# Kernel optimization log

Hardware: AMD Instinct MI355X
Metric: run time of the kernel (lower is better)

The kernel has to match this reference:

```python
import jax, jax.numpy as jnp
import numpy as np
from jax import lax

# 8-neighbor zero-pad offsets as (left, right, top, bottom), matching nn.ZeroPad2d args
PADS = [(0, 2, 0, 2), (1, 1, 0, 2), (2, 0, 0, 2), (0, 2, 1, 1),
        (2, 0, 1, 1), (0, 2, 2, 0), (1, 1, 2, 0), (2, 0, 2, 0)]
BN_EPS = 1e-5


def conv2d(x, w, pad):
    return lax.conv_general_dilated(x, w, (1, 1), [(pad, pad), (pad, pad)],
                                    dimension_numbers=('NCHW', 'OIHW', 'NCHW'))


def batchnorm(x, gamma, beta, mean, var):
    inv = gamma * lax.rsqrt(var + BN_EPS)
    return x * inv[None, :, None, None] + (beta - mean * inv)[None, :, None, None]


def resize_bilinear(x, oh, ow):
    # F.interpolate(mode='bilinear', align_corners=False)
    n, c, h, w = x.shape
    ys = jnp.clip((jnp.arange(oh, dtype=x.dtype) + 0.5) * (h / oh) - 0.5, 0.0, None)
    xs = jnp.clip((jnp.arange(ow, dtype=x.dtype) + 0.5) * (w / ow) - 0.5, 0.0, None)
    y0 = jnp.floor(ys); x0 = jnp.floor(xs)
    wy = (ys - y0)[:, None]; wx = (xs - x0)[None, :]
    y0i = jnp.clip(y0.astype(jnp.int32), 0, h - 1)
    y1i = jnp.clip(y0i + 1, 0, h - 1)
    x0i = jnp.clip(x0.astype(jnp.int32), 0, w - 1)
    x1i = jnp.clip(x0i + 1, 0, w - 1)
    r0 = x[:, :, y0i, :]; r1 = x[:, :, y1i, :]
    top = r0[:, :, :, x0i] * (1 - wx) + r0[:, :, :, x1i] * wx
    bot = r1[:, :, :, x0i] * (1 - wx) + r1[:, :, :, x1i] * wx
    return top * (1 - wy) + bot * wy


def lrwarp_error(left, disp, right):
    # Warp right image toward left using horizontal disparity (bilinear,
    # zero padding outside), then per-channel absolute photometric error.
    n, c, h, w = right.shape
    xs = jnp.arange(w, dtype=disp.dtype)[None, None, None, :] - disp  # [n,1,h,w]
    x0 = jnp.floor(xs)
    frac = xs - x0
    x0i = x0.astype(jnp.int32)
    x1i = x0i + 1
    v0 = ((x0i >= 0) & (x0i < w)).astype(right.dtype)
    v1 = ((x1i >= 0) & (x1i < w)).astype(right.dtype)
    x0c = jnp.broadcast_to(jnp.clip(x0i, 0, w - 1), (n, c, h, w))
    x1c = jnp.broadcast_to(jnp.clip(x1i, 0, w - 1), (n, c, h, w))
    g0 = jnp.take_along_axis(right, x0c, axis=3) * v0
    g1 = jnp.take_along_axis(right, x1c, axis=3) * v1
    warped = g0 * (1 - frac) + g1 * frac
    return jnp.abs(left - warped)


def setup_inputs() -> dict:
    key = jax.random.key(0)
    ks = jax.random.split(key, 16)
    N, H, W = 8, 256, 256
    inp = {
        'normal_estimation': jax.random.normal(ks[0], (N, 3, H, W), jnp.float32),
        'left_image': jax.random.uniform(ks[1], (N, 3, 512, 512), jnp.float32),
        'right_image': jax.random.uniform(ks[2], (N, 3, 512, 512), jnp.float32),
        'coarse_disparity': jax.random.uniform(ks[3], (N, 1, H, W), jnp.float32),
        'w1': jax.random.normal(ks[4], (32, 12, 3, 3), jnp.float32) * 0.1,
        'g1': jnp.ones((32,), jnp.float32), 'b1': jnp.zeros((32,), jnp.float32),
        'm1': jax.random.normal(ks[5], (32,), jnp.float32) * 0.01,
        'v1': jax.random.uniform(ks[6], (32,), jnp.float32, 0.5, 1.5),
        'w2': jax.random.normal(ks[7], (64, 32, 3, 3), jnp.float32) * 0.1,
        'g2': jnp.ones((64,), jnp.float32), 'b2': jnp.zeros((64,), jnp.float32),
        'm2': jax.random.normal(ks[8], (64,), jnp.float32) * 0.01,
        'v2': jax.random.uniform(ks[9], (64,), jnp.float32, 0.5, 1.5),
        'w3': jax.random.normal(ks[10], (8, 64, 1, 1), jnp.float32) * 0.1,
    }
    return inp


def _forward(normal_estimation, left_image, right_image, coarse_disparity,
             w1, g1, b1, m1, v1, w2, g2, b2, m2, v2, w3):
    H, W = coarse_disparity.shape[-2], coarse_disparity.shape[-1]
    cur_l = resize_bilinear(left_image, H, W)
    cur_r = resize_bilinear(right_image, H, W)
    disp_err = lrwarp_error(cur_l, coarse_disparity, cur_r)
    feats = jnp.concatenate([normal_estimation, cur_l, cur_r, disp_err], axis=1)
    x = jax.nn.relu(batchnorm(conv2d(feats, w1, 1), g1, b1, m1, v1))
    x = jax.nn.relu(batchnorm(conv2d(x, w2, 1), g2, b2, m2, v2))
    aff = jax.nn.relu(conv2d(x, w3, 0))  # [N,8,H,W]
    gate_p = jnp.stack([jnp.pad(aff[:, k], ((0, 0), (t, b), (l, r)))
                        for k, (l, r, t, b) in enumerate(PADS)], axis=1)
    d = coarse_disparity[:, 0]
    disp_p = jnp.stack([jnp.pad(d, ((0, 0), (t, b), (l, r)))
                        for (l, r, t, b) in PADS], axis=1)
    gate = jax.nn.softmax(gate_p, axis=1)
    prop = jnp.sum(gate * disp_p, axis=1, keepdims=True)[:, :, 1:-1, 1:-1]
    return prop * 0.3 + coarse_disparity * 0.7


def reference(normal_estimation, left_image, right_image, coarse_disparity,
              w1, g1, b1, m1, v1, w2, g2, b2, m2, v2, w3):
    return _forward(normal_estimation, left_image, right_image, coarse_disparity,
                    w1, g1, b1, m1, v1, w2, g2, b2, m2, v2, w3)
```

## Files before the change

kernel.cpp:

```cpp
#include <hip/hip_runtime.h>
#include <math.h>

#define NB 8
#define HH 256
#define WW 256
#define HW (HH*WW)

#define OFF_FEATS 0UL
#define OFF_X1B   16777216UL
#define OFF_AFFB  50331648UL
#define OFF_W1FB  67108864UL
#define OFF_B1FB  67121152UL
#define OFF_W2FB  67121280UL
#define OFF_B2FB  67158144UL

typedef short  short8 __attribute__((ext_vector_type(8)));
typedef ushort u16x8  __attribute__((ext_vector_type(8)));
typedef ushort u16x4  __attribute__((ext_vector_type(4)));
typedef float  f32x4  __attribute__((ext_vector_type(4)));

__device__ __forceinline__ ushort f2bf(float x) {
  uint u = __float_as_uint(x);
  return (ushort)((u + 0x7FFFu + ((u >> 16) & 1u)) >> 16);
}
__device__ __forceinline__ float bf2f(ushort h) {
  uint u = ((uint)h) << 16;
  return __uint_as_float(u);
}

__global__ __launch_bounds__(256) void prep_weights(
    const float* __restrict__ w1, const float* __restrict__ g1,
    const float* __restrict__ b1, const float* __restrict__ m1,
    const float* __restrict__ v1,
    const float* __restrict__ w2, const float* __restrict__ g2,
    const float* __restrict__ b2, const float* __restrict__ m2,
    const float* __restrict__ v2,
    char* __restrict__ wsb) {
  int idx = blockIdx.x * 256 + threadIdx.x;
  ushort* w1f = (ushort*)(wsb + OFF_W1FB);
  float* b1f  = (float*)(wsb + OFF_B1FB);
  ushort* w2f = (ushort*)(wsb + OFF_W2FB);
  float* b2f  = (float*)(wsb + OFF_B2FB);
  if (idx < 6144) {
    int jj = idx & 7;
    int lane = (idx >> 3) & 63;
    int mt = (idx >> 9) & 1;
    int s = idx >> 10;
    int ky = s >> 1, t = s & 1;
    int q = lane >> 4, lx = lane & 15;
    int k = q * 8 + jj;
    int dcol = k >> 4, ch = k & 15;
    int kx = t * 2 + dcol;
    int out = mt * 16 + lx;
    float inv = g1[out] / sqrtf(v1[out] + 1e-5f);
    float val = (ch < 12 && kx < 3) ? w1[((out * 12 + ch) * 3 + ky) * 3 + kx] * inv : 0.f;
    w1f[idx] = f2bf(val);
  }
  int j = idx - 6144;
  if (j >= 0 && j < 18432) {
    int kk   = j >> 11;
    int nt   = (j >> 9) & 3;
    int lane = (j >> 3) & 63;
    int jj   = j & 7;
    int q  = lane >> 4, lx = lane & 15;
    int cin = q * 8 + jj;
    int out = nt * 16 + lx;
    float inv = g2[out] / sqrtf(v2[out] + 1e-5f);
    w2f[j] = f2bf(w2[(out * 32 + cin) * 9 + kk] * inv);
    if (kk == 0 && q == 0 && jj == 0) b2f[out] = b2[out] - m2[out] * inv;
  }
  int k2 = idx - 24576;
  if (k2 >= 0 && k2 < 32) {
    float inv = g1[k2] / sqrtf(v1[k2] + 1e-5f);
    b1f[k2] = b1[k2] - m1[k2] * inv;
  }
}

__device__ __forceinline__ float avg4(const float* __restrict__ img, int n, int c,
                                      int i2, int x) {
  const float* p = img + ((size_t)(n * 3 + c) * 512 + i2) * 512 + 2 * x;
  float2 a = *(const float2*)p;
  float2 b = *(const float2*)(p + 512);
  return 0.25f * (a.x + a.y + b.x + b.y);
}

__global__ __launch_bounds__(256) void build_feats(
    const float* __restrict__ normal, const float* __restrict__ left,
    const float* __restrict__ right, const float* __restrict__ disp,
    char* __restrict__ wsb) {
  int gid = blockIdx.x * 256 + threadIdx.x;
  int n = gid / HW;
  int r = gid - n * HW;
  int i = r / WW;
  int j = r - i * WW;
  ushort* feats = (ushort*)(wsb + OFF_FEATS);
  ushort tmp[16];
  int i2 = 2 * i;
#pragma unroll
  for (int c = 0; c < 3; ++c)
    tmp[c] = f2bf(normal[(size_t)(n * 3 + c) * HW + i * WW + j]);
  float cl[3];
#pragma unroll
  for (int c = 0; c < 3; ++c) {
    cl[c] = avg4(left, n, c, i2, j);
    float cr = avg4(right, n, c, i2, j);
    tmp[3 + c] = f2bf(cl[c]);
    tmp[6 + c] = f2bf(cr);
  }
  float d = disp[n * HW + i * WW + j];
  float xs = (float)j - d;
  float x0f = floorf(xs);
  float fr = xs - x0f;
  int x0 = (int)x0f;
  int x1 = x0 + 1;
  float v0 = (x0 >= 0 && x0 < WW) ? 1.f : 0.f;
  float v1 = (x1 >= 0 && x1 < WW) ? 1.f : 0.f;
  int x0c = min(max(x0, 0), WW - 1);
  int x1c = min(max(x1, 0), WW - 1);
#pragma unroll
  for (int c = 0; c < 3; ++c) {
    float gg0 = avg4(right, n, c, i2, x0c) * v0;
    float gg1 = avg4(right, n, c, i2, x1c) * v1;
    float warped = gg0 * (1.f - fr) + gg1 * fr;
    tmp[9 + c] = f2bf(fabsf(cl[c] - warped));
  }
#pragma unroll
  for (int c = 12; c < 16; ++c) tmp[c] = 0;
  size_t ob = ((size_t)gid) * 16;
  *(u16x8*)&feats[ob] = *(u16x8*)&tmp[0];
  *(u16x8*)&feats[ob + 8] = *(u16x8*)&tmp[8];
}

__global__ __launch_bounds__(256) void conv1_kernel(char* __restrict__ wsb) {
  __shared__ ushort tile[688 * 8];
  const ushort* __restrict__ feats = (const ushort*)(wsb + OFF_FEATS);
  const short8* __restrict__ w1fv = (const short8*)(wsb + OFF_W1FB);
  const float* __restrict__ b1f = (const float*)(wsb + OFF_B1FB);
  ushort* x1 = (ushort*)(wsb + OFF_X1B);
  int blk = blockIdx.x;
  int n = blk >> 8;
  int t = blk & 255;
  int ty0 = (t >> 4) << 4;
  int tx0 = (t & 15) << 4;
  int tid = threadIdx.x;
  for (int e = tid; e < 684; e += 256) {
    int row = e / 38;
    int rem = e - row * 38;
    int col = rem >> 1;
    int cc = rem & 1;
    int gy = ty0 + row - 1, gx = tx0 + col - 1;
    u16x8 v = (u16x8)0;
    if (gy >= 0 && gy < HH && gx >= 0 && gx < WW)
      v = *(const u16x8*)&feats[(((size_t)(n * 256 + gy)) * 256 + gx) * 16 + cc * 8];
    int slot = e ^ ((e >> 3) & 7);
    *(u16x8*)&tile[slot * 8] = v;
  }
  __syncthreads();
  int lane = tid & 63;
  int wid = tid >> 6;
  int q = lane >> 4;
  int lx = lane & 15;
  short8 aw[2][6];
#pragma unroll
  for (int s = 0; s < 6; ++s)
#pragma unroll
    for (int mt = 0; mt < 2; ++mt) aw[mt][s] = w1fv[(s * 2 + mt) * 64 + lane];
  f32x4 acc[4][2];
#pragma unroll
  for (int rowt = 0; rowt < 4; ++rowt)
#pragma unroll
    for (int mt = 0; mt < 2; ++mt) acc[rowt][mt] = (f32x4)0.f;
#pragma unroll
  for (int s = 0; s < 6; ++s) {
    int ky = s >> 1;
    int kxs = (s & 1) * 2;
#pragma unroll
    for (int rowt = 0; rowt < 4; ++rowt) {
      int prow = wid * 4 + rowt + ky;
      int G = (prow * 19 + lx + kxs + (q >> 1)) * 2 + (q & 1);
      int slot = G ^ ((G >> 3) & 7);
      short8 b = *(const short8*)&tile[slot * 8];
      acc[rowt][0] = __builtin_amdgcn_mfma_f32_16x16x32_bf16(aw[0][s], b, acc[rowt][0], 0, 0, 0);
      acc[rowt][1] = __builtin_amdgcn_mfma_f32_16x16x32_bf16(aw[1][s], b, acc[rowt][1], 0, 0, 0);
    }
  }
#pragma unroll
  for (int rowt = 0; rowt < 4; ++rowt) {
    int gy = ty0 + wid * 4 + rowt;
    int gx = tx0 + lx;
    size_t pb = (((size_t)(n * 256 + gy)) * 256 + gx) * 32;
#pragma unroll
    for (int mt = 0; mt < 2; ++mt) {
      u16x4 pack;
#pragma unroll
      for (int r = 0; r < 4; ++r) {
        int ch = mt * 16 + q * 4 + r;
        pack[r] = f2bf(fmaxf(acc[rowt][mt][r] + b1f[ch], 0.f));
      }
      *(u16x4*)&x1[pb + mt * 16 + q * 4] = pack;
    }
  }
}

__global__ __launch_bounds__(256) void conv2_kernel(char* __restrict__ wsb,
                                                    const float* __restrict__ w3) {
  __shared__ ushort smem[256 * 68];
  const ushort* __restrict__ x1 = (const ushort*)(wsb + OFF_X1B);
  const short8* __restrict__ w2fv = (const short8*)(wsb + OFF_W2FB);
  const float* __restrict__ b2f = (const float*)(wsb + OFF_B2FB);
  float* aff = (float*)(wsb + OFF_AFFB);

  int blk = blockIdx.x;
  int n = blk >> 8;
  int t = blk & 255;
  int ty0 = (t >> 4) << 4;
  int tx0 = (t & 15) << 4;
  int tid = threadIdx.x;

  for (int e = tid; e < 1296; e += 256) {
    int p = e >> 2;
    int c = e & 3;
    int y = p / 18;
    int x = p - y * 18;
    int gy = ty0 + y - 1, gx = tx0 + x - 1;
    u16x8 val = (u16x8)0;
    if (gy >= 0 && gy < HH && gx >= 0 && gx < WW)
      val = *(const u16x8*)&x1[(((size_t)(n * 256 + gy)) * 256 + gx) * 32 + c * 8];
    *(u16x8*)&smem[p * 36 + c * 8] = val;
  }
  __syncthreads();

  int lane = tid & 63;
  int wid = tid >> 6;
  int q = lane >> 4;
  int lx = lane & 15;

  f32x4 acc[4][4];
#pragma unroll
  for (int mt = 0; mt < 4; ++mt)
#pragma unroll
    for (int nt = 0; nt < 4; ++nt) acc[mt][nt] = (f32x4)0.f;

#pragma unroll
  for (int kk = 0; kk < 9; ++kk) {
    int ky = kk / 3, kx = kk - ky * 3;
    short8 a[4], b[4];
#pragma unroll
    for (int mt = 0; mt < 4; ++mt) {
      int row = wid * 4 + mt;
      a[mt] = *(const short8*)&smem[((row + ky) * 18 + lx + kx) * 36 + q * 8];
    }
#pragma unroll
    for (int nt = 0; nt < 4; ++nt) b[nt] = w2fv[(kk * 4 + nt) * 64 + lane];
#pragma unroll
    for (int mt = 0; mt < 4; ++mt)
#pragma unroll
      for (int nt = 0; nt < 4; ++nt)
        acc[mt][nt] = __builtin_amdgcn_mfma_f32_16x16x32_bf16(a[mt], b[nt], acc[mt][nt], 0, 0, 0);
  }

  __syncthreads();
#pragma unroll
  for (int nt = 0; nt < 4; ++nt) {
    float bias = b2f[nt * 16 + lx];
#pragma unroll
    for (int mt = 0; mt < 4; ++mt) {
      int row = wid * 4 + mt;
#pragma unroll
      for (int r = 0; r < 4; ++r) {
        int p = row * 16 + q * 4 + r;
        float v = fmaxf(acc[mt][nt][r] + bias, 0.f);
        smem[p * 68 + nt * 16 + lx] = f2bf(v);
      }
    }
  }
  __syncthreads();

  int p = tid;
  float x2v[64];
#pragma unroll
  for (int cb = 0; cb < 8; ++cb) {
    u16x8 hv = *(const u16x8*)&smem[p * 68 + cb * 8];
#pragma unroll
    for (int jj = 0; jj < 8; ++jj) x2v[cb * 8 + jj] = bf2f(hv[jj]);
  }
  int py = ty0 + (p >> 4), px = tx0 + (p & 15);
  size_t obase = (size_t)n * 8 * HW + (size_t)py * WW + px;
#pragma unroll
  for (int k = 0; k < 8; ++k) {
    float s = 0.f;
#pragma unroll
    for (int c = 0; c < 64; ++c) s = fmaf(x2v[c], w3[k * 64 + c], s);
    aff[obase + (size_t)k * HW] = fmaxf(s, 0.f);
  }
}

__global__ __launch_bounds__(256) void final_kernel(const float* __restrict__ disp,
                                                    const char* __restrict__ wsb,
                                                    float* __restrict__ out) {
  int gid = blockIdx.x * 256 + threadIdx.x;
  int n = gid / HW;
  int r = gid - n * HW;
  int i = r / WW;
  int j = r - i * WW;
  const float* aff = (const float*)(wsb + OFF_AFFB);
  const int dy[8] = {1, 1, 1, 0, 0, -1, -1, -1};
  const int dx[8] = {1, 0, -1, 1, -1, 1, 0, -1};
  float g[8], dv[8];
#pragma unroll
  for (int k = 0; k < 8; ++k) {
    int y = i + dy[k], x = j + dx[k];
    bool ok = (y >= 0 && y < HH && x >= 0 && x < WW);
    g[k] = ok ? aff[(size_t)(n * 8 + k) * HW + y * WW + x] : 0.f;
    dv[k] = ok ? disp[n * HW + y * WW + x] : 0.f;
  }
  float m = g[0];
#pragma unroll
  for (int k = 1; k < 8; ++k) m = fmaxf(m, g[k]);
  float se = 0.f, sed = 0.f;
#pragma unroll
  for (int k = 0; k < 8; ++k) {
    float e = __expf(g[k] - m);
    se += e;
    sed += e * dv[k];
  }
  float dc = disp[n * HW + i * WW + j];
  out[gid] = 0.3f * (sed / se) + 0.7f * dc;
}

extern "C" void kernel_launch(void* const* d_in, const int* in_sizes, int n_in,
                              void* d_out, int out_size, void* d_ws, size_t ws_size,
                              hipStream_t stream) {
  const float* normal = (const float*)d_in[0];
  const float* left   = (const float*)d_in[1];
  const float* right  = (const float*)d_in[2];
  const float* disp   = (const float*)d_in[3];
  const float* w1 = (const float*)d_in[4];
  const float* g1 = (const float*)d_in[5];
  const float* b1 = (const float*)d_in[6];
  const float* m1 = (const float*)d_in[7];
  const float* v1 = (const float*)d_in[8];
  const float* w2 = (const float*)d_in[9];
  const float* g2 = (const float*)d_in[10];
  const float* b2 = (const float*)d_in[11];
  const float* m2 = (const float*)d_in[12];
  const float* v2 = (const float*)d_in[13];
  const float* w3 = (const float*)d_in[14];
  char* wsb  = (char*)d_ws;
  float* out = (float*)d_out;

  hipLaunchKernelGGL(prep_weights, dim3(97), dim3(256), 0, stream,
                     w1, g1, b1, m1, v1, w2, g2, b2, m2, v2, wsb);
  hipLaunchKernelGGL(build_feats, dim3(2048), dim3(256), 0, stream,
                     normal, left, right, disp, wsb);
  hipLaunchKernelGGL(conv1_kernel, dim3(2048), dim3(256), 0, stream, wsb);
  hipLaunchKernelGGL(conv2_kernel, dim3(2048), dim3(256), 0, stream, wsb, w3);
  hipLaunchKernelGGL(final_kernel, dim3(2048), dim3(256), 0, stream, disp, wsb, out);
}
```

Before: 181.1 us.

## Fold weight prep into feature kernel, use MFMA for 1x1 conv, store bf16 affinities

The weight-preparation kernel is merged into build_feats as extra blocks, which removes one launch. The final 1x1 conv (64->8) in conv2 now runs on bf16 MFMA with pre-packed w3 fragments instead of a per-thread scalar FMA loop. Affinities are stored as bf16, halving that intermediate's traffic. conv1 also hoists its weight loads before the tile barrier and preloads B fragments so they are reused across kernel rows. The costs are reduced precision for the affinity logits, extra register pressure in conv1, and MFMA lanes wasted on the padded output channels.

```diff
diff --git a/kernel.cpp b/kernel.cpp
--- a/kernel.cpp
+++ b/kernel.cpp
@@ -9,10 +9,11 @@
 #define OFF_FEATS 0UL
 #define OFF_X1B   16777216UL
 #define OFF_AFFB  50331648UL
-#define OFF_W1FB  67108864UL
-#define OFF_B1FB  67121152UL
-#define OFF_W2FB  67121280UL
-#define OFF_B2FB  67158144UL
+#define OFF_W1FB  58720256UL
+#define OFF_B1FB  58732544UL
+#define OFF_W2FB  58732672UL
+#define OFF_B2FB  58769536UL
+#define OFF_W3FB  58769792UL
 
 typedef short  short8 __attribute__((ext_vector_type(8)));
 typedef ushort u16x8  __attribute__((ext_vector_type(8)));
@@ -26,54 +27,6 @@
 __device__ __forceinline__ float bf2f(ushort h) {
   uint u = ((uint)h) << 16;
   return __uint_as_float(u);
-}
-
-__global__ __launch_bounds__(256) void prep_weights(
-    const float* __restrict__ w1, const float* __restrict__ g1,
-    const float* __restrict__ b1, const float* __restrict__ m1,
-    const float* __restrict__ v1,
-    const float* __restrict__ w2, const float* __restrict__ g2,
-    const float* __restrict__ b2, const float* __restrict__ m2,
-    const float* __restrict__ v2,
-    char* __restrict__ wsb) {
-  int idx = blockIdx.x * 256 + threadIdx.x;
-  ushort* w1f = (ushort*)(wsb + OFF_W1FB);
-  float* b1f  = (float*)(wsb + OFF_B1FB);
-  ushort* w2f = (ushort*)(wsb + OFF_W2FB);
-  float* b2f  = (float*)(wsb + OFF_B2FB);
-  if (idx < 6144) {
-    int jj = idx & 7;
-    int lane = (idx >> 3) & 63;
-    int mt = (idx >> 9) & 1;
-    int s = idx >> 10;
-    int ky = s >> 1, t = s & 1;
-    int q = lane >> 4, lx = lane & 15;
-    int k = q * 8 + jj;
-    int dcol = k >> 4, ch = k & 15;
-    int kx = t * 2 + dcol;
-    int out = mt * 16 + lx;
-    float inv = g1[out] / sqrtf(v1[out] + 1e-5f);
-    float val = (ch < 12 && kx < 3) ? w1[((out * 12 + ch) * 3 + ky) * 3 + kx] * inv : 0.f;
-    w1f[idx] = f2bf(val);
-  }
-  int j = idx - 6144;
-  if (j >= 0 && j < 18432) {
-    int kk   = j >> 11;
-    int nt   = (j >> 9) & 3;
-    int lane = (j >> 3) & 63;
-    int jj   = j & 7;
-    int q  = lane >> 4, lx = lane & 15;
-    int cin = q * 8 + jj;
-    int out = nt * 16 + lx;
-    float inv = g2[out] / sqrtf(v2[out] + 1e-5f);
-    w2f[j] = f2bf(w2[(out * 32 + cin) * 9 + kk] * inv);
-    if (kk == 0 && q == 0 && jj == 0) b2f[out] = b2[out] - m2[out] * inv;
-  }
-  int k2 = idx - 24576;
-  if (k2 >= 0 && k2 < 32) {
-    float inv = g1[k2] / sqrtf(v1[k2] + 1e-5f);
-    b1f[k2] = b1[k2] - m1[k2] * inv;
-  }
 }
 
 __device__ __forceinline__ float avg4(const float* __restrict__ img, int n, int c,
@@ -87,7 +40,64 @@
 __global__ __launch_bounds__(256) void build_feats(
     const float* __restrict__ normal, const float* __restrict__ left,
     const float* __restrict__ right, const float* __restrict__ disp,
+    const float* __restrict__ w1, const float* __restrict__ g1,
+    const float* __restrict__ b1, const float* __restrict__ m1,
+    const float* __restrict__ v1,
+    const float* __restrict__ w2, const float* __restrict__ g2,
+    const float* __restrict__ b2, const float* __restrict__ m2,
+    const float* __restrict__ v2, const float* __restrict__ w3,
     char* __restrict__ wsb) {
+  if (blockIdx.x >= 2048) {
+    int idx = (blockIdx.x - 2048) * 256 + threadIdx.x;
+    ushort* w1f = (ushort*)(wsb + OFF_W1FB);
+    float* b1f  = (float*)(wsb + OFF_B1FB);
+    ushort* w2f = (ushort*)(wsb + OFF_W2FB);
+    float* b2f  = (float*)(wsb + OFF_B2FB);
+    ushort* w3f = (ushort*)(wsb + OFF_W3FB);
+    if (idx < 6144) {
+      int jj = idx & 7;
+      int lane = (idx >> 3) & 63;
+      int mt = (idx >> 9) & 1;
+      int s = idx >> 10;
+      int ky = s >> 1, t = s & 1;
+      int q = lane >> 4, lx = lane & 15;
+      int k = q * 8 + jj;
+      int dcol = k >> 4, ch = k & 15;
+      int kx = t * 2 + dcol;
+      int out = mt * 16 + lx;
+      float inv = g1[out] / sqrtf(v1[out] + 1e-5f);
+      float val = (ch < 12 && kx < 3) ? w1[((out * 12 + ch) * 3 + ky) * 3 + kx] * inv : 0.f;
+      w1f[idx] = f2bf(val);
+    }
+    int j = idx - 6144;
+    if (j >= 0 && j < 18432) {
+      int kk   = j >> 11;
+      int nt   = (j >> 9) & 3;
+      int lane = (j >> 3) & 63;
+      int jj   = j & 7;
+      int q  = lane >> 4, lx = lane & 15;
+      int cin = q * 8 + jj;
+      int out = nt * 16 + lx;
+      float inv = g2[out] / sqrtf(v2[out] + 1e-5f);
+      w2f[j] = f2bf(w2[(out * 32 + cin) * 9 + kk] * inv);
+      if (kk == 0 && q == 0 && jj == 0) b2f[out] = b2[out] - m2[out] * inv;
+    }
+    int k2 = idx - 24576;
+    if (k2 >= 0 && k2 < 32) {
+      float inv = g1[k2] / sqrtf(v1[k2] + 1e-5f);
+      b1f[k2] = b1[k2] - m1[k2] * inv;
+    }
+    int k3 = idx - 24608;
+    if (k3 >= 0 && k3 < 1024) {
+      int jj = k3 & 7;
+      int lane = (k3 >> 3) & 63;
+      int slice = k3 >> 9;
+      int q = lane >> 4, lx = lane & 15;
+      int ch = slice * 32 + q * 8 + jj;
+      w3f[k3] = (lx < 8) ? f2bf(w3[lx * 64 + ch]) : (ushort)0;
+    }
+    return;
+  }
   int gid = blockIdx.x * 256 + threadIdx.x;
   int n = gid / HW;
   int r = gid - n * HW;
@@ -111,16 +121,16 @@
   float xs = (float)j - d;
   float x0f = floorf(xs);
   float fr = xs - x0f;
-  int x0 = (int)x0f;
-  int x1 = x0 + 1;
-  float v0 = (x0 >= 0 && x0 < WW) ? 1.f : 0.f;
-  float v1 = (x1 >= 0 && x1 < WW) ? 1.f : 0.f;
-  int x0c = min(max(x0, 0), WW - 1);
-  int x1c = min(max(x1, 0), WW - 1);
+  int ix0 = (int)x0f;
+  int ix1 = ix0 + 1;
+  float vm0 = (ix0 >= 0 && ix0 < WW) ? 1.f : 0.f;
+  float vm1 = (ix1 >= 0 && ix1 < WW) ? 1.f : 0.f;
+  int x0c = min(max(ix0, 0), WW - 1);
+  int x1c = min(max(ix1, 0), WW - 1);
 #pragma unroll
   for (int c = 0; c < 3; ++c) {
-    float gg0 = avg4(right, n, c, i2, x0c) * v0;
-    float gg1 = avg4(right, n, c, i2, x1c) * v1;
+    float gg0 = avg4(right, n, c, i2, x0c) * vm0;
+    float gg1 = avg4(right, n, c, i2, x1c) * vm1;
     float warped = gg0 * (1.f - fr) + gg1 * fr;
     tmp[9 + c] = f2bf(fabsf(cl[c] - warped));
   }
@@ -143,6 +153,15 @@
   int ty0 = (t >> 4) << 4;
   int tx0 = (t & 15) << 4;
   int tid = threadIdx.x;
+  int lane = tid & 63;
+  int wid = tid >> 6;
+  int q = lane >> 4;
+  int lx = lane & 15;
+  short8 aw[2][6];
+#pragma unroll
+  for (int s = 0; s < 6; ++s)
+#pragma unroll
+    for (int mt = 0; mt < 2; ++mt) aw[mt][s] = w1fv[(s * 2 + mt) * 64 + lane];
   for (int e = tid; e < 684; e += 256) {
     int row = e / 38;
     int rem = e - row * 38;
@@ -156,15 +175,16 @@
     *(u16x8*)&tile[slot * 8] = v;
   }
   __syncthreads();
-  int lane = tid & 63;
-  int wid = tid >> 6;
-  int q = lane >> 4;
-  int lx = lane & 15;
-  short8 aw[2][6];
-#pragma unroll
-  for (int s = 0; s < 6; ++s)
-#pragma unroll
-    for (int mt = 0; mt < 2; ++mt) aw[mt][s] = w1fv[(s * 2 + mt) * 64 + lane];
+  short8 bfrag[6][2];
+#pragma unroll
+  for (int dr = 0; dr < 6; ++dr)
+#pragma unroll
+    for (int tt = 0; tt < 2; ++tt) {
+      int prow = wid * 4 + dr;
+      int G = (prow * 19 + lx + tt * 2 + (q >> 1)) * 2 + (q & 1);
+      int slot = G ^ ((G >> 3) & 7);
+      bfrag[dr][tt] = *(const short8*)&tile[slot * 8];
+    }
   f32x4 acc[4][2];
 #pragma unroll
   for (int rowt = 0; rowt < 4; ++rowt)
@@ -173,13 +193,10 @@
 #pragma unroll
   for (int s = 0; s < 6; ++s) {
     int ky = s >> 1;
-    int kxs = (s & 1) * 2;
+    int tt = s & 1;
 #pragma unroll
     for (int rowt = 0; rowt < 4; ++rowt) {
-      int prow = wid * 4 + rowt + ky;
-      int G = (prow * 19 + lx + kxs + (q >> 1)) * 2 + (q & 1);
-      int slot = G ^ ((G >> 3) & 7);
-      short8 b = *(const short8*)&tile[slot * 8];
+      short8 b = bfrag[rowt + ky][tt];
       acc[rowt][0] = __builtin_amdgcn_mfma_f32_16x16x32_bf16(aw[0][s], b, acc[rowt][0], 0, 0, 0);
       acc[rowt][1] = __builtin_amdgcn_mfma_f32_16x16x32_bf16(aw[1][s], b, acc[rowt][1], 0, 0, 0);
     }
@@ -202,13 +219,13 @@
   }
 }
 
-__global__ __launch_bounds__(256) void conv2_kernel(char* __restrict__ wsb,
-                                                    const float* __restrict__ w3) {
+__global__ __launch_bounds__(256) void conv2_kernel(char* __restrict__ wsb) {
   __shared__ ushort smem[256 * 68];
   const ushort* __restrict__ x1 = (const ushort*)(wsb + OFF_X1B);
   const short8* __restrict__ w2fv = (const short8*)(wsb + OFF_W2FB);
   const float* __restrict__ b2f = (const float*)(wsb + OFF_B2FB);
-  float* aff = (float*)(wsb + OFF_AFFB);
+  const short8* __restrict__ w3fv = (const short8*)(wsb + OFF_W3FB);
+  ushort* aff = (ushort*)(wsb + OFF_AFFB);
 
   int blk = blockIdx.x;
   int n = blk >> 8;
@@ -216,6 +233,14 @@
   int ty0 = (t >> 4) << 4;
   int tx0 = (t & 15) << 4;
   int tid = threadIdx.x;
+  int lane = tid & 63;
+  int wid = tid >> 6;
+  int q = lane >> 4;
+  int lx = lane & 15;
+
+  short8 bw3[2];
+  bw3[0] = w3fv[lane];
+  bw3[1] = w3fv[64 + lane];
 
   for (int e = tid; e < 1296; e += 256) {
     int p = e >> 2;
@@ -230,11 +255,6 @@
   }
   __syncthreads();
 
-  int lane = tid & 63;
-  int wid = tid >> 6;
-  int q = lane >> 4;
-  int lx = lane & 15;
-
   f32x4 acc[4][4];
 #pragma unroll
   for (int mt = 0; mt < 4; ++mt)
@@ -276,22 +296,28 @@
   }
   __syncthreads();
 
-  int p = tid;
-  float x2v[64];
-#pragma unroll
-  for (int cb = 0; cb < 8; ++cb) {
-    u16x8 hv = *(const u16x8*)&smem[p * 68 + cb * 8];
-#pragma unroll
-    for (int jj = 0; jj < 8; ++jj) x2v[cb * 8 + jj] = bf2f(hv[jj]);
-  }
-  int py = ty0 + (p >> 4), px = tx0 + (p & 15);
-  size_t obase = (size_t)n * 8 * HW + (size_t)py * WW + px;
-#pragma unroll
-  for (int k = 0; k < 8; ++k) {
-    float s = 0.f;
-#pragma unroll
-    for (int c = 0; c < 64; ++c) s = fmaf(x2v[c], w3[k * 64 + c], s);
-    aff[obase + (size_t)k * HW] = fmaxf(s, 0.f);
+  f32x4 acc3[4];
+#pragma unroll
+  for (int mt = 0; mt < 4; ++mt) acc3[mt] = (f32x4)0.f;
+#pragma unroll
+  for (int mt = 0; mt < 4; ++mt) {
+    int p = wid * 64 + mt * 16 + lx;
+#pragma unroll
+    for (int s = 0; s < 2; ++s) {
+      short8 a3 = *(const short8*)&smem[p * 68 + s * 32 + q * 8];
+      acc3[mt] = __builtin_amdgcn_mfma_f32_16x16x32_bf16(a3, bw3[s], acc3[mt], 0, 0, 0);
+    }
+  }
+  if (lx < 8) {
+#pragma unroll
+    for (int mt = 0; mt < 4; ++mt) {
+      int py = ty0 + wid * 4 + mt;
+      int px = tx0 + q * 4;
+      u16x4 pk;
+#pragma unroll
+      for (int r = 0; r < 4; ++r) pk[r] = f2bf(fmaxf(acc3[mt][r], 0.f));
+      *(u16x4*)&aff[((size_t)(n * 8 + lx)) * HW + (size_t)py * WW + px] = pk;
+    }
   }
 }
 
@@ -303,7 +329,7 @@
   int r = gid - n * HW;
   int i = r / WW;
   int j = r - i * WW;
-  const float* aff = (const float*)(wsb + OFF_AFFB);
+  const ushort* aff = (const ushort*)(wsb + OFF_AFFB);
   const int dy[8] = {1, 1, 1, 0, 0, -1, -1, -1};
   const int dx[8] = {1, 0, -1, 1, -1, 1, 0, -1};
   float g[8], dv[8];
@@ -311,7 +337,7 @@
   for (int k = 0; k < 8; ++k) {
     int y = i + dy[k], x = j + dx[k];
     bool ok = (y >= 0 && y < HH && x >= 0 && x < WW);
-    g[k] = ok ? aff[(size_t)(n * 8 + k) * HW + y * WW + x] : 0.f;
+    g[k] = ok ? bf2f(aff[(size_t)(n * 8 + k) * HW + y * WW + x]) : 0.f;
     dv[k] = ok ? disp[n * HW + y * WW + x] : 0.f;
   }
   float m = g[0];
@@ -349,11 +375,10 @@
   char* wsb  = (char*)d_ws;
   float* out = (float*)d_out;
 
-  hipLaunchKernelGGL(prep_weights, dim3(97), dim3(256), 0, stream,
-                     w1, g1, b1, m1, v1, w2, g2, b2, m2, v2, wsb);
-  hipLaunchKernelGGL(build_feats, dim3(2048), dim3(256), 0, stream,
-                     normal, left, right, disp, wsb);
+  hipLaunchKernelGGL(build_feats, dim3(2149), dim3(256), 0, stream,
+                     normal, left, right, disp,
+                     w1, g1, b1, m1, v1, w2, g2, b2, m2, v2, w3, wsb);
   hipLaunchKernelGGL(conv1_kernel, dim3(2048), dim3(256), 0, stream, wsb);
-  hipLaunchKernelGGL(conv2_kernel, dim3(2048), dim3(256), 0, stream, wsb, w3);
+  hipLaunchKernelGGL(conv2_kernel, dim3(2048), dim3(256), 0, stream, wsb);
   hipLaunchKernelGGL(final_kernel, dim3(2048), dim3(256), 0, stream, disp, wsb, out);
 }
```

Result: faster. 167.3 us (-7.6%).
